# Optimization experiments

Measured on AMD Instinct MI355X. Metric: run time of the kernel, lower is better.

## Reference

```python
import jax, jax.numpy as jnp
import numpy as np

H, W = 30, 30
D = 256
MAX_OBJECTS = 16
SENT = H * W  # sentinel label for background / invalid slots


def label_components(grid):
    """4-connected same-color connected-component labeling.
    grid: [B,H,W] int32. Returns labels [B,H,W] where each foreground cell
    carries the minimum linear index of its component (== raster-scan BFS
    discovery order of the torch code), SENT for background."""
    B = grid.shape[0]
    lin = jnp.arange(H * W, dtype=jnp.int32).reshape(1, H, W)
    fg = grid > 0
    init = jnp.where(fg, lin, SENT).astype(jnp.int32)
    big = jnp.int32(SENT)

    def nbr_min(lab):
        lp = jnp.pad(lab, ((0, 0), (1, 1), (1, 1)), constant_values=SENT)
        gp = jnp.pad(grid, ((0, 0), (1, 1), (1, 1)), constant_values=-1)
        m = lab
        for di, dj in ((-1, 0), (1, 0), (0, -1), (0, 1)):
            ls = lp[:, 1 + di:1 + di + H, 1 + dj:1 + dj + W]
            gs = gp[:, 1 + di:1 + di + H, 1 + dj:1 + dj + W]
            m = jnp.minimum(m, jnp.where(gs == grid, ls, big))
        return jnp.where(fg, m, big)

    def cond(s):
        return s[1]

    def body(s):
        lab, _ = s
        new = nbr_min(lab)
        # pointer jumping: label <- min(label, label[label]) accelerates convergence
        flat = new.reshape(B, H * W)
        jumped = jnp.take_along_axis(flat, jnp.clip(flat, 0, H * W - 1), axis=1)
        flat = jnp.where(flat < SENT, jnp.minimum(flat, jumped), SENT)
        new = flat.reshape(B, H, W)
        return new, jnp.any(new != lab)

    labels, _ = jax.lax.while_loop(cond, body, (init, jnp.array(True)))
    return labels


def extract_objects(grid, labels):
    """Per-slot (color, y, x, h, w, valid), each [B, MAX_OBJECTS]."""
    B = grid.shape[0]
    HW = H * W
    lin = jnp.arange(HW, dtype=jnp.int32)
    rows, cols = lin // W, lin % W
    lab = labels.reshape(B, HW)
    ns = HW + 1  # extra segment collects background
    seg = jnp.where(lab < SENT, lab, SENT)
    rmin = jax.vmap(lambda s: jax.ops.segment_min(rows, s, num_segments=ns))(seg)
    rmax = jax.vmap(lambda s: jax.ops.segment_max(rows, s, num_segments=ns))(seg)
    cmin = jax.vmap(lambda s: jax.ops.segment_min(cols, s, num_segments=ns))(seg)
    cmax = jax.vmap(lambda s: jax.ops.segment_max(cols, s, num_segments=ns))(seg)
    # component roots, in raster order == BFS discovery order; keep first K
    root = jnp.where((lab == lin[None, :]) & (lab < SENT), lin[None, :], SENT)
    order = jnp.sort(root, axis=1)[:, :MAX_OBJECTS]
    valid = order < SENT
    idx = jnp.clip(order, 0, HW - 1)
    bi = jnp.arange(B)[:, None]
    y = jnp.clip(rmin[bi, idx], 0, H - 1)
    x = jnp.clip(cmin[bi, idx], 0, W - 1)
    y2 = jnp.clip(rmax[bi, idx] + 1, y + 1, H)
    x2 = jnp.clip(cmax[bi, idx] + 1, x + 1, W)
    color = grid.reshape(B, HW)[bi, idx]
    return color, y, x, y2 - y, x2 - x, valid


def forward(grid_emb, structure_rep, W1, b1, W2, b2, Wp, bp, gamma, beta, ortho_scale, objs):
    color, y, x, h, w, valid = objs
    B = grid_emb.shape[0]
    bi = jnp.arange(B)[:, None]
    # summed-area table -> bbox mean-pool of grid_emb in O(1) per object
    S = jnp.pad(jnp.cumsum(jnp.cumsum(grid_emb, axis=1), axis=2),
                ((0, 0), (1, 0), (1, 0), (0, 0)))
    y2, x2 = y + h, x + w
    pool = S[bi, y2, x2] - S[bi, y, x2] - S[bi, y2, x] + S[bi, y, x]
    pool = pool / (h * w).astype(grid_emb.dtype)[..., None]       # [B,K,D]
    bbox = jnp.stack([color / 9.0, x / W, y / H, w / W, h / H], axis=-1).astype(grid_emb.dtype)
    combined = jnp.concatenate([pool, bbox], axis=-1)              # [B,K,D+5]
    hdn = jax.nn.gelu(jnp.einsum('bkf,fd->bkd', combined, W1) + b1, approximate=False)
    obj = jnp.einsum('bkd,de->bke', hdn, W2) + b2
    obj = jnp.where(valid[..., None], obj, 0.0)  # pad slots are zero embeddings
    # OrthogonalProjector with structure broadcast = mean over structure slots
    s = structure_rep.mean(axis=1, keepdims=True)                  # [B,1,D]
    sn = s / jnp.maximum(jnp.linalg.norm(s, axis=-1, keepdims=True), 1e-8)
    dot = (obj * sn).sum(axis=-1, keepdims=True)
    co = (obj - dot * sn) * ortho_scale
    co = jnp.einsum('bkd,de->bke', co, Wp) + bp
    mu = co.mean(axis=-1, keepdims=True)
    var = ((co - mu) ** 2).mean(axis=-1, keepdims=True)
    return (co - mu) / jnp.sqrt(var + 1e-5) * gamma + beta


def setup_inputs() -> dict:
    key = jax.random.key(0)
    ks = jax.random.split(key, 6)
    B, K_STRUCT = 128, 8
    grid_emb = jax.random.normal(ks[0], (B, H, W, D), dtype=jnp.float32)
    grid = jax.random.randint(ks[1], (B, H, W), 0, 10, dtype=jnp.int32)
    structure_rep = jax.random.normal(ks[2], (B, K_STRUCT, D), dtype=jnp.float32)
    sc = 0.02
    W1 = jax.random.normal(ks[3], (D + 5, D), dtype=jnp.float32) * sc
    b1 = jnp.zeros((D,), jnp.float32)
    W2 = jax.random.normal(ks[4], (D, D), dtype=jnp.float32) * sc
    b2 = jnp.zeros((D,), jnp.float32)
    Wp = jax.random.normal(ks[5], (D, D), dtype=jnp.float32) * sc
    bp = jnp.zeros((D,), jnp.float32)
    gamma = jnp.ones((D,), jnp.float32)
    beta = jnp.zeros((D,), jnp.float32)
    ortho_scale = jnp.ones((1,), jnp.float32)
    return dict(grid_emb=grid_emb, grid=grid, structure_rep=structure_rep,
                W1=W1, b1=b1, W2=W2, b2=b2, Wp=Wp, bp=bp,
                gamma=gamma, beta=beta, ortho_scale=ortho_scale)


def reference(grid_emb, grid, structure_rep, W1, b1, W2, b2, Wp, bp, gamma, beta, ortho_scale):
    labels = label_components(grid)
    objs = extract_objects(grid, labels)
    return forward(grid_emb, structure_rep, W1, b1, W2, b2, Wp, bp, gamma, beta, ortho_scale, objs)
```

## Files before the change

kernel.cpp:

```cpp
#include <hip/hip_runtime.h>
#include <math.h>

#define HH 30
#define WWID 30
#define HW 900
#define SENTV 900
#define DD 256
#define MAXK 16
#define AK 264

typedef __attribute__((ext_vector_type(8))) short short8b;
typedef __attribute__((ext_vector_type(4))) float f32x4;

__device__ __forceinline__ float gelu_exact(float x) {
    return 0.5f * x * (1.0f + erff(x * 0.70710678118654752440f));
}

__device__ __forceinline__ unsigned short f2bf(float x) {
    unsigned int u = __float_as_uint(x);
    u += 0x7FFFu + ((u >> 16) & 1u);
    return (unsigned short)(u >> 16);
}

__global__ __launch_bounds__(256) void conv_w(
    const float* __restrict__ W1, const float* __restrict__ W2,
    const float* __restrict__ Wp, unsigned short* __restrict__ ws)
{
    int f = blockIdx.x * 256 + threadIdx.x;
    int m = f >> 13;
    int rem = f & 8191;
    int ntile = rem >> 9;
    int kl = rem & 511;
    int ktile = kl >> 6;
    int lane = kl & 63;
    const float* W = (m == 0) ? W1 : (m == 1) ? W2 : Wp;
    int k0 = ktile * 32 + (lane >> 4) * 8;
    int n  = ntile * 16 + (lane & 15);
    unsigned short* dst = ws + (size_t)m * 65536 +
                          ((size_t)(ntile * 8 + ktile) * 64 + lane) * 8;
    #pragma unroll
    for (int i = 0; i < 8; ++i) dst[i] = f2bf(W[(size_t)(k0 + i) * DD + n]);
}

__device__ __forceinline__ void mfma_pass16(
    const unsigned short (* __restrict__ ab)[AK],
    const unsigned short* __restrict__ wm,
    f32x4* acc, int cl, int tx, int wv)
{
    short8b afr[8];
    #pragma unroll
    for (int kt = 0; kt < 8; ++kt)
        afr[kt] = *(const short8b*)&ab[cl][kt * 32 + (tx >> 4) * 8];
    const short8b* base = (const short8b*)wm;
    short8b bfr[8];
    #pragma unroll
    for (int kt = 0; kt < 8; ++kt)
        bfr[kt] = base[(wv * 8 + kt) * 64 + tx];
    #pragma unroll
    for (int kt = 0; kt < 8; ++kt)
        *acc = __builtin_amdgcn_mfma_f32_16x16x32_bf16(afr[kt], bfr[kt], *acc, 0, 0, 0);
}

__global__ __launch_bounds__(1024, 4) void ccce_main(
    const float* __restrict__ grid_emb,
    const int* __restrict__ grid,
    const float* __restrict__ structure_rep,
    const unsigned short* __restrict__ wsw,
    const float* __restrict__ W1, const float* __restrict__ b1,
    const float* __restrict__ b2, const float* __restrict__ bp,
    const float* __restrict__ gvec, const float* __restrict__ bvec,
    const float* __restrict__ ortho_scale,
    float* __restrict__ out, int KS)
{
    const int b   = blockIdx.x;
    const int tid = threadIdx.x;
    const int tx  = tid & 63;
    const int wv  = tid >> 6;
    const int cl  = tx & 15;
    const int g   = tx >> 4;

    __shared__ int color_s[HW];
    __shared__ int lab_s[HW];
    __shared__ int slot_of[HW];
    __shared__ int root_s[MAXK];
    __shared__ int nroot_s;
    __shared__ int by0[MAXK], by1[MAXK], bx0[MAXK], bx1[MAXK];
    __shared__ __align__(16) unsigned short a0[16][AK];
    __shared__ __align__(16) unsigned short a1[16][AK];
    __shared__ __align__(16) float sn_s[DD];
    __shared__ float red_s[4];
    __shared__ float feats_s[16][5];
    __shared__ float dred[16][16];
    __shared__ float lred[16][16][2];

    const int4* gp = (const int4*)(grid + (size_t)b * HW);
    int4 gld;
    if (tid < 225) gld = gp[tid];

    const bool do_s = (tid < DD);
    float sl0=0.f,sl1=0.f,sl2=0.f,sl3=0.f,sl4=0.f,sl5=0.f,sl6=0.f,sl7=0.f,s_gen=0.f;
    {
        const float* sr = structure_rep + (size_t)b * KS * DD + tid;
        if (do_s) {
            if (KS == 8) {
                sl0 = sr[0*DD]; sl1 = sr[1*DD]; sl2 = sr[2*DD]; sl3 = sr[3*DD];
                sl4 = sr[4*DD]; sl5 = sr[5*DD]; sl6 = sr[6*DD]; sl7 = sr[7*DD];
            } else {
                for (int j = 0; j < KS; ++j) s_gen += sr[(size_t)j * DD];
            }
        }
    }

    if (tid < 225) {
        int i = tid * 4;
        color_s[i+0] = gld.x; lab_s[i+0] = (gld.x > 0) ? (i+0) : SENTV;
        color_s[i+1] = gld.y; lab_s[i+1] = (gld.y > 0) ? (i+1) : SENTV;
        color_s[i+2] = gld.z; lab_s[i+2] = (gld.z > 0) ? (i+2) : SENTV;
        color_s[i+3] = gld.w; lab_s[i+3] = (gld.w > 0) ? (i+3) : SENTV;
    }
    __syncthreads();

    const int li = tid;
    int nm = 0;
    if (li < HW) {
        int c = color_s[li];
        if (c > 0) {
            int r = li / WWID, cc = li - (li / WWID) * WWID;
            nm = 16;
            if (r > 0       && color_s[li - WWID] == c) nm |= 1;
            if (r < HH - 1  && color_s[li + WWID] == c) nm |= 2;
            if (cc > 0      && color_s[li - 1]    == c) nm |= 4;
            if (cc < WWID-1 && color_s[li + 1]    == c) nm |= 8;
        }
    }

    for (;;) {
        if (nm & 16) {
            int m = lab_s[li];
            if (nm & 1) m = min(m, lab_s[li - WWID]);
            if (nm & 2) m = min(m, lab_s[li + WWID]);
            if (nm & 4) m = min(m, lab_s[li - 1]);
            if (nm & 8) m = min(m, lab_s[li + 1]);
            m = min(m, lab_s[m]);
            m = min(m, lab_s[m]);
            if (m < lab_s[li]) lab_s[li] = m;
        }
        __syncthreads();
        int ch = 0;
        if (nm & 16) {
            int m = lab_s[li];
            if (nm & 1) m = min(m, lab_s[li - WWID]);
            if (nm & 2) m = min(m, lab_s[li + WWID]);
            if (nm & 4) m = min(m, lab_s[li - 1]);
            if (nm & 8) m = min(m, lab_s[li + 1]);
            m = min(m, lab_s[m]);
            m = min(m, lab_s[m]);
            if (m < lab_s[li]) { lab_s[li] = m; ch = 1; }
        }
        if (__syncthreads_count(ch) == 0) break;
    }

    if (tid < 64) {
        int base = 0;
        for (int chk = 0; chk < 15; ++chk) {
            int cell = chk * 64 + tid;
            bool isr = (cell < HW) && (color_s[cell] > 0) && (lab_s[cell] == cell);
            unsigned long long mask = __ballot(isr);
            int rank = base + __popcll(mask & ((1ull << tid) - 1ull));
            if (isr && rank < MAXK) root_s[rank] = cell;
            base += __popcll(mask);
        }
        if (tid == 0) nroot_s = base;
    } else {
        for (int i = tid - 64; i < HW; i += 960) slot_of[i] = -1;
        if (tid >= 960 && tid < 960 + MAXK) {
            int k = tid - 960;
            by0[k] = HH; by1[k] = -1; bx0[k] = WWID; bx1[k] = -1;
        }
    }
    __syncthreads();

    const int nval = min(nroot_s, MAXK);
    if (tid < nval) slot_of[root_s[tid]] = tid;
    __syncthreads();

    if (nm & 16) {
        int s = slot_of[lab_s[li]];
        if (s >= 0) {
            int r = li / WWID, cc = li - (li / WWID) * WWID;
            atomicMin(&by0[s], r); atomicMax(&by1[s], r);
            atomicMin(&bx0[s], cc); atomicMax(&bx1[s], cc);
        }
    }

    float s_mean = (KS == 8)
        ? (sl0 + sl1 + sl2 + sl3 + sl4 + sl5 + sl6 + sl7) * 0.125f
        : s_gen * (1.0f / (float)KS);
    {
        float ss = s_mean * s_mean;
        #pragma unroll
        for (int off = 32; off > 0; off >>= 1) ss += __shfl_xor(ss, off);
        if (tx == 0 && wv < 4) red_s[wv] = ss;
    }
    __syncthreads();

    if (do_s) {
        float nrm = sqrtf(red_s[0] + red_s[1] + red_s[2] + red_s[3]);
        sn_s[tid] = s_mean / fmaxf(nrm, 1e-8f);
    }

    {
        const int slot = wv;
        const int v_ok = (slot < nval) ? 1 : 0;
        const int c0 = tx * 4;
        float4 pv = make_float4(0.f, 0.f, 0.f, 0.f);
        int y = 0, x = 0, h = 1, w = 1, col = 0;
        if (v_ok) {
            y = by0[slot]; x = bx0[slot];
            h = by1[slot] + 1 - y; w = bx1[slot] + 1 - x;
            col = color_s[root_s[slot]];
            const int n = h * w;
            const float* bp_ = grid_emb + ((size_t)(b * HH + y) * WWID + x) * DD + c0;
            float4 sum = make_float4(0.f, 0.f, 0.f, 0.f);
            for (int base2 = 0; base2 < n; base2 += 8) {
                float4 v[8];
                #pragma unroll
                for (int t = 0; t < 8; ++t) {
                    int ii = base2 + t;
                    if (ii < n) {
                        int yy = ii / w, xx = ii - yy * w;
                        v[t] = *(const float4*)(bp_ + ((size_t)yy * WWID + xx) * DD);
                    }
                }
                #pragma unroll
                for (int t = 0; t < 8; ++t) {
                    int ii = base2 + t;
                    if (ii < n) { sum.x += v[t].x; sum.y += v[t].y; sum.z += v[t].z; sum.w += v[t].w; }
                }
            }
            float inv = 1.0f / (float)n;
            pv.x = sum.x * inv; pv.y = sum.y * inv; pv.z = sum.z * inv; pv.w = sum.w * inv;
        }
        unsigned int p0 = (unsigned int)f2bf(pv.x) | ((unsigned int)f2bf(pv.y) << 16);
        unsigned int p1 = (unsigned int)f2bf(pv.z) | ((unsigned int)f2bf(pv.w) << 16);
        *(unsigned int*)&a0[wv][c0]     = p0;
        *(unsigned int*)&a0[wv][c0 + 2] = p1;
        if (tx < 5) {
            float f = 0.f;
            if (v_ok) {
                switch (tx) {
                    case 0: f = (float)col / 9.0f; break;
                    case 1: f = (float)x  / 30.0f; break;
                    case 2: f = (float)y  / 30.0f; break;
                    case 3: f = (float)w  / 30.0f; break;
                    case 4: f = (float)h  / 30.0f; break;
                }
            }
            feats_s[wv][tx] = f;
        }
    }
    __syncthreads();

    {
        f32x4 acc = {0, 0, 0, 0};
        mfma_pass16(a0, wsw, &acc, cl, tx, wv);
        const int col = wv * 16 + cl;
        float b1v = b1[col];
        float tw[5];
        #pragma unroll
        for (int jj = 0; jj < 5; ++jj) tw[jj] = W1[(size_t)(256 + jj) * DD + col];
        #pragma unroll
        for (int j = 0; j < 4; ++j) {
            int row = g * 4 + j;
            float s = acc[j] + b1v;
            #pragma unroll
            for (int jj = 0; jj < 5; ++jj) s += feats_s[row][jj] * tw[jj];
            a1[row][col] = f2bf(gelu_exact(s));
        }
        __syncthreads();
    }

    {
        f32x4 acc = {0, 0, 0, 0};
        mfma_pass16(a1, wsw + 65536, &acc, cl, tx, wv);
        const int col = wv * 16 + cl;
        float b2v = b2[col];
        float snc = sn_s[col];
        float obj[4];
        float pd[4];
        #pragma unroll
        for (int j = 0; j < 4; ++j) {
            int row = g * 4 + j;
            float vm = (row < nval) ? 1.f : 0.f;
            obj[j] = (acc[j] + b2v) * vm;
            pd[j] = obj[j] * snc;
        }
        #pragma unroll
        for (int off = 1; off < 16; off <<= 1) {
            #pragma unroll
            for (int j = 0; j < 4; ++j) pd[j] += __shfl_xor(pd[j], off);
        }
        if (cl == 0) {
            #pragma unroll
            for (int j = 0; j < 4; ++j) dred[wv][g * 4 + j] = pd[j];
        }
        __syncthreads();
        float osc = ortho_scale[0];
        #pragma unroll
        for (int j = 0; j < 4; ++j) {
            int row = g * 4 + j;
            float p = 0.f;
            #pragma unroll
            for (int w = 0; w < 16; ++w) p += dred[w][row];
            a0[row][col] = f2bf((obj[j] - p * snc) * osc);
        }
        __syncthreads();
    }

    {
        f32x4 acc = {0, 0, 0, 0};
        mfma_pass16(a0, wsw + 2 * 65536, &acc, cl, tx, wv);
        const int col = wv * 16 + cl;
        float bpv = bp[col];
        float v[4], S[4], Q[4];
        #pragma unroll
        for (int j = 0; j < 4; ++j) {
            v[j] = acc[j] + bpv;
            S[j] = v[j];
            Q[j] = v[j] * v[j];
        }
        #pragma unroll
        for (int off = 1; off < 16; off <<= 1) {
            #pragma unroll
            for (int j = 0; j < 4; ++j) {
                S[j] += __shfl_xor(S[j], off);
                Q[j] += __shfl_xor(Q[j], off);
            }
        }
        if (cl == 0) {
            #pragma unroll
            for (int j = 0; j < 4; ++j) {
                lred[wv][g * 4 + j][0] = S[j];
                lred[wv][g * 4 + j][1] = Q[j];
            }
        }
        __syncthreads();
        float gvc = gvec[col], bvc = bvec[col];
        #pragma unroll
        for (int j = 0; j < 4; ++j) {
            int row = g * 4 + j;
            float Ss = 0.f, Qq = 0.f;
            #pragma unroll
            for (int w = 0; w < 16; ++w) { Ss += lred[w][row][0]; Qq += lred[w][row][1]; }
            float mu   = Ss * (1.0f / 256.0f);
            float var  = fmaxf(Qq * (1.0f / 256.0f) - mu * mu, 0.0f);
            float rstd = 1.0f / sqrtf(var + 1e-5f);
            out[((size_t)(b * MAXK + row)) * DD + col] = (v[j] - mu) * rstd * gvc + bvc;
        }
    }
}

extern "C" void kernel_launch(void* const* d_in, const int* in_sizes, int n_in,
                              void* d_out, int out_size, void* d_ws, size_t ws_size,
                              hipStream_t stream) {
    const float* grid_emb = (const float*)d_in[0];
    const int*   grid     = (const int*)d_in[1];
    const float* srep     = (const float*)d_in[2];
    const float* W1v = (const float*)d_in[3];
    const float* b1v = (const float*)d_in[4];
    const float* W2v = (const float*)d_in[5];
    const float* b2v = (const float*)d_in[6];
    const float* Wpv = (const float*)d_in[7];
    const float* bpv = (const float*)d_in[8];
    const float* gv  = (const float*)d_in[9];
    const float* bv  = (const float*)d_in[10];
    const float* osv = (const float*)d_in[11];
    float* out = (float*)d_out;

    const int B  = in_sizes[1] / HW;
    const int KS = in_sizes[2] / (B * DD);

    unsigned short* wsw = (unsigned short*)d_ws;
    hipLaunchKernelGGL(conv_w, dim3(96), dim3(256), 0, stream,
                       W1v, W2v, Wpv, wsw);
    hipLaunchKernelGGL(ccce_main, dim3(B), dim3(1024), 0, stream,
                       grid_emb, grid, srep, wsw, W1v, b1v, b2v, bpv,
                       gv, bv, osv, out, KS);
}
```

Before: 27.81 us.

## Fuse weight conversion into main kernel via cooperative launch and grid sync

```diff
diff --git a/kernel.cpp b/kernel.cpp
--- a/kernel.cpp
+++ b/kernel.cpp
@@ -1,5 +1,8 @@
 #include <hip/hip_runtime.h>
+#include <hip/hip_cooperative_groups.h>
 #include <math.h>
+
+namespace cg = cooperative_groups;
 
 #define HH 30
 #define WWID 30
@@ -8,6 +11,7 @@
 #define DD 256
 #define MAXK 16
 #define AK 264
+#define NFRAG 24576
 
 typedef __attribute__((ext_vector_type(8))) short short8b;
 typedef __attribute__((ext_vector_type(4))) float f32x4;
@@ -20,26 +24,6 @@
     unsigned int u = __float_as_uint(x);
     u += 0x7FFFu + ((u >> 16) & 1u);
     return (unsigned short)(u >> 16);
-}
-
-__global__ __launch_bounds__(256) void conv_w(
-    const float* __restrict__ W1, const float* __restrict__ W2,
-    const float* __restrict__ Wp, unsigned short* __restrict__ ws)
-{
-    int f = blockIdx.x * 256 + threadIdx.x;
-    int m = f >> 13;
-    int rem = f & 8191;
-    int ntile = rem >> 9;
-    int kl = rem & 511;
-    int ktile = kl >> 6;
-    int lane = kl & 63;
-    const float* W = (m == 0) ? W1 : (m == 1) ? W2 : Wp;
-    int k0 = ktile * 32 + (lane >> 4) * 8;
-    int n  = ntile * 16 + (lane & 15);
-    unsigned short* dst = ws + (size_t)m * 65536 +
-                          ((size_t)(ntile * 8 + ktile) * 64 + lane) * 8;
-    #pragma unroll
-    for (int i = 0; i < 8; ++i) dst[i] = f2bf(W[(size_t)(k0 + i) * DD + n]);
 }
 
 __device__ __forceinline__ void mfma_pass16(
@@ -65,9 +49,11 @@
     const float* __restrict__ grid_emb,
     const int* __restrict__ grid,
     const float* __restrict__ structure_rep,
-    const unsigned short* __restrict__ wsw,
-    const float* __restrict__ W1, const float* __restrict__ b1,
-    const float* __restrict__ b2, const float* __restrict__ bp,
+    unsigned short* __restrict__ wsw,
+    const float* __restrict__ W1, const float* __restrict__ W2,
+    const float* __restrict__ Wp,
+    const float* __restrict__ b1, const float* __restrict__ b2,
+    const float* __restrict__ bp,
     const float* __restrict__ gvec, const float* __restrict__ bvec,
     const float* __restrict__ ortho_scale,
     float* __restrict__ out, int KS)
@@ -111,12 +97,45 @@
         }
     }
 
+    {
+        const int fpb = (NFRAG + gridDim.x - 1) / gridDim.x;
+        for (int t = tid; t < fpb; t += 1024) {
+            int f = b * fpb + t;
+            if (f < NFRAG) {
+                int m = f >> 13;
+                int rem = f & 8191;
+                int ntile = rem >> 9;
+                int kl = rem & 511;
+                int ktile = kl >> 6;
+                int lane = kl & 63;
+                const float* W = (m == 0) ? W1 : (m == 1) ? W2 : Wp;
+                int k0 = ktile * 32 + (lane >> 4) * 8;
+                int n  = ntile * 16 + (lane & 15);
+                const float* src = W + (size_t)k0 * DD + n;
+                float v0 = src[0*DD], v1 = src[1*DD], v2 = src[2*DD], v3 = src[3*DD];
+                float v4 = src[4*DD], v5 = src[5*DD], v6 = src[6*DD], v7 = src[7*DD];
+                short8b frag;
+                frag[0] = (short)f2bf(v0); frag[1] = (short)f2bf(v1);
+                frag[2] = (short)f2bf(v2); frag[3] = (short)f2bf(v3);
+                frag[4] = (short)f2bf(v4); frag[5] = (short)f2bf(v5);
+                frag[6] = (short)f2bf(v6); frag[7] = (short)f2bf(v7);
+                *(short8b*)(wsw + (size_t)m * 65536 +
+                            ((size_t)(ntile * 8 + ktile) * 64 + lane) * 8) = frag;
+            }
+        }
+    }
+
     if (tid < 225) {
         int i = tid * 4;
         color_s[i+0] = gld.x; lab_s[i+0] = (gld.x > 0) ? (i+0) : SENTV;
         color_s[i+1] = gld.y; lab_s[i+1] = (gld.y > 0) ? (i+1) : SENTV;
         color_s[i+2] = gld.z; lab_s[i+2] = (gld.z > 0) ? (i+2) : SENTV;
         color_s[i+3] = gld.w; lab_s[i+3] = (gld.w > 0) ? (i+3) : SENTV;
+    }
+    if (tid < HW) slot_of[tid] = -1;
+    if (tid >= 1000 && tid < 1000 + MAXK) {
+        int k = tid - 1000;
+        by0[k] = HH; by1[k] = -1; bx0[k] = WWID; bx1[k] = -1;
     }
     __syncthreads();
 
@@ -167,22 +186,14 @@
             bool isr = (cell < HW) && (color_s[cell] > 0) && (lab_s[cell] == cell);
             unsigned long long mask = __ballot(isr);
             int rank = base + __popcll(mask & ((1ull << tid) - 1ull));
-            if (isr && rank < MAXK) root_s[rank] = cell;
+            if (isr && rank < MAXK) { root_s[rank] = cell; slot_of[cell] = rank; }
             base += __popcll(mask);
         }
         if (tid == 0) nroot_s = base;
-    } else {
-        for (int i = tid - 64; i < HW; i += 960) slot_of[i] = -1;
-        if (tid >= 960 && tid < 960 + MAXK) {
-            int k = tid - 960;
-            by0[k] = HH; by1[k] = -1; bx0[k] = WWID; bx1[k] = -1;
-        }
     }
     __syncthreads();
 
     const int nval = min(nroot_s, MAXK);
-    if (tid < nval) slot_of[root_s[tid]] = tid;
-    __syncthreads();
 
     if (nm & 16) {
         int s = slot_of[lab_s[li]];
@@ -261,6 +272,9 @@
     }
     __syncthreads();
 
+    __threadfence();
+    cg::this_grid().sync();
+
     {
         f32x4 acc = {0, 0, 0, 0};
         mfma_pass16(a0, wsw, &acc, cl, tx, wv);
@@ -377,13 +391,15 @@
     const float* osv = (const float*)d_in[11];
     float* out = (float*)d_out;
 
-    const int B  = in_sizes[1] / HW;
-    const int KS = in_sizes[2] / (B * DD);
-
+    int B  = in_sizes[1] / HW;
+    int KS = in_sizes[2] / (B * DD);
     unsigned short* wsw = (unsigned short*)d_ws;
-    hipLaunchKernelGGL(conv_w, dim3(96), dim3(256), 0, stream,
-                       W1v, W2v, Wpv, wsw);
-    hipLaunchKernelGGL(ccce_main, dim3(B), dim3(1024), 0, stream,
-                       grid_emb, grid, srep, wsw, W1v, b1v, b2v, bpv,
-                       gv, bv, osv, out, KS);
+
+    void* args[] = { (void*)&grid_emb, (void*)&grid, (void*)&srep, (void*)&wsw,
+                     (void*)&W1v, (void*)&W2v, (void*)&Wpv,
+                     (void*)&b1v, (void*)&b2v, (void*)&bpv,
+                     (void*)&gv, (void*)&bv, (void*)&osv,
+                     (void*)&out, (void*)&KS };
+    hipLaunchCooperativeKernel((void*)ccce_main, dim3(B), dim3(1024),
+                               args, 0, stream);
 }
```

Measured after the change: 89.64 us. +222.4%, slower.

## Fuse weight bf16 conversion into main kernel and prefetch fragments into registers

Applied to the files above, without the earlier changes.

```diff
diff --git a/kernel.cpp b/kernel.cpp
--- a/kernel.cpp
+++ b/kernel.cpp
@@ -11,6 +11,7 @@
 
 typedef __attribute__((ext_vector_type(8))) short short8b;
 typedef __attribute__((ext_vector_type(4))) float f32x4;
+typedef __attribute__((ext_vector_type(4))) unsigned int uint4v;
 
 __device__ __forceinline__ float gelu_exact(float x) {
     return 0.5f * x * (1.0f + erff(x * 0.70710678118654752440f));
@@ -22,52 +23,58 @@
     return (unsigned short)(u >> 16);
 }
 
-__global__ __launch_bounds__(256) void conv_w(
-    const float* __restrict__ W1, const float* __restrict__ W2,
-    const float* __restrict__ Wp, unsigned short* __restrict__ ws)
+__device__ __forceinline__ unsigned int cvt_pk_bf16(float a, float b) {
+    unsigned int d;
+    asm("v_cvt_pk_bf16_f32 %0, %1, %2" : "=v"(d) : "v"(a), "v"(b));
+    return d;
+}
+
+__device__ __forceinline__ void load_wfrags(
+    const float* __restrict__ W, int wv, int cl, int g, short8b wf[8])
 {
-    int f = blockIdx.x * 256 + threadIdx.x;
-    int m = f >> 13;
-    int rem = f & 8191;
-    int ntile = rem >> 9;
-    int kl = rem & 511;
-    int ktile = kl >> 6;
-    int lane = kl & 63;
-    const float* W = (m == 0) ? W1 : (m == 1) ? W2 : Wp;
-    int k0 = ktile * 32 + (lane >> 4) * 8;
-    int n  = ntile * 16 + (lane & 15);
-    unsigned short* dst = ws + (size_t)m * 65536 +
-                          ((size_t)(ntile * 8 + ktile) * 64 + lane) * 8;
+    const float* src = W + (size_t)(g * 8) * DD + (wv * 16 + cl);
     #pragma unroll
-    for (int i = 0; i < 8; ++i) dst[i] = f2bf(W[(size_t)(k0 + i) * DD + n]);
-}
-
-__device__ __forceinline__ void mfma_pass16(
+    for (int half = 0; half < 2; ++half) {
+        float v[4][8];
+        #pragma unroll
+        for (int kt = 0; kt < 4; ++kt) {
+            #pragma unroll
+            for (int i = 0; i < 8; ++i)
+                v[kt][i] = src[(size_t)((half * 4 + kt) * 32 + i) * DD];
+        }
+        #pragma unroll
+        for (int kt = 0; kt < 4; ++kt) {
+            union { uint4v u; short8b s; } cv;
+            cv.u[0] = cvt_pk_bf16(v[kt][0], v[kt][1]);
+            cv.u[1] = cvt_pk_bf16(v[kt][2], v[kt][3]);
+            cv.u[2] = cvt_pk_bf16(v[kt][4], v[kt][5]);
+            cv.u[3] = cvt_pk_bf16(v[kt][6], v[kt][7]);
+            wf[half * 4 + kt] = cv.s;
+        }
+    }
+}
+
+__device__ __forceinline__ void mfma_pass_reg(
     const unsigned short (* __restrict__ ab)[AK],
-    const unsigned short* __restrict__ wm,
-    f32x4* acc, int cl, int tx, int wv)
+    const short8b wf[8], f32x4* acc, int cl, int g)
 {
     short8b afr[8];
     #pragma unroll
     for (int kt = 0; kt < 8; ++kt)
-        afr[kt] = *(const short8b*)&ab[cl][kt * 32 + (tx >> 4) * 8];
-    const short8b* base = (const short8b*)wm;
-    short8b bfr[8];
+        afr[kt] = *(const short8b*)&ab[cl][kt * 32 + g * 8];
     #pragma unroll
     for (int kt = 0; kt < 8; ++kt)
-        bfr[kt] = base[(wv * 8 + kt) * 64 + tx];
-    #pragma unroll
-    for (int kt = 0; kt < 8; ++kt)
-        *acc = __builtin_amdgcn_mfma_f32_16x16x32_bf16(afr[kt], bfr[kt], *acc, 0, 0, 0);
+        *acc = __builtin_amdgcn_mfma_f32_16x16x32_bf16(afr[kt], wf[kt], *acc, 0, 0, 0);
 }
 
 __global__ __launch_bounds__(1024, 4) void ccce_main(
     const float* __restrict__ grid_emb,
     const int* __restrict__ grid,
     const float* __restrict__ structure_rep,
-    const unsigned short* __restrict__ wsw,
-    const float* __restrict__ W1, const float* __restrict__ b1,
-    const float* __restrict__ b2, const float* __restrict__ bp,
+    const float* __restrict__ W1, const float* __restrict__ W2,
+    const float* __restrict__ Wp,
+    const float* __restrict__ b1, const float* __restrict__ b2,
+    const float* __restrict__ bp,
     const float* __restrict__ gvec, const float* __restrict__ bvec,
     const float* __restrict__ ortho_scale,
     float* __restrict__ out, int KS)
@@ -118,6 +125,11 @@
         color_s[i+2] = gld.z; lab_s[i+2] = (gld.z > 0) ? (i+2) : SENTV;
         color_s[i+3] = gld.w; lab_s[i+3] = (gld.w > 0) ? (i+3) : SENTV;
     }
+    if (tid < HW) slot_of[tid] = -1;
+    if (tid >= 1000 && tid < 1000 + MAXK) {
+        int k = tid - 1000;
+        by0[k] = HH; by1[k] = -1; bx0[k] = WWID; bx1[k] = -1;
+    }
     __syncthreads();
 
     const int li = tid;
@@ -134,6 +146,9 @@
         }
     }
 
+    short8b wfA[8];
+    load_wfrags(W1, wv, cl, g, wfA);
+
     for (;;) {
         if (nm & 16) {
             int m = lab_s[li];
@@ -167,22 +182,14 @@
             bool isr = (cell < HW) && (color_s[cell] > 0) && (lab_s[cell] == cell);
             unsigned long long mask = __ballot(isr);
             int rank = base + __popcll(mask & ((1ull << tid) - 1ull));
-            if (isr && rank < MAXK) root_s[rank] = cell;
+            if (isr && rank < MAXK) { root_s[rank] = cell; slot_of[cell] = rank; }
             base += __popcll(mask);
         }
         if (tid == 0) nroot_s = base;
-    } else {
-        for (int i = tid - 64; i < HW; i += 960) slot_of[i] = -1;
-        if (tid >= 960 && tid < 960 + MAXK) {
-            int k = tid - 960;
-            by0[k] = HH; by1[k] = -1; bx0[k] = WWID; bx1[k] = -1;
-        }
     }
     __syncthreads();
 
     const int nval = min(nroot_s, MAXK);
-    if (tid < nval) slot_of[root_s[tid]] = tid;
-    __syncthreads();
 
     if (nm & 16) {
         int s = slot_of[lab_s[li]];
@@ -259,11 +266,14 @@
             feats_s[wv][tx] = f;
         }
     }
+
+    short8b wfB[8];
+    load_wfrags(W2, wv, cl, g, wfB);
     __syncthreads();
 
     {
         f32x4 acc = {0, 0, 0, 0};
-        mfma_pass16(a0, wsw, &acc, cl, tx, wv);
+        mfma_pass_reg(a0, wfA, &acc, cl, g);
         const int col = wv * 16 + cl;
         float b1v = b1[col];
         float tw[5];
@@ -280,9 +290,11 @@
         __syncthreads();
     }
 
+    short8b wfC[8];
     {
         f32x4 acc = {0, 0, 0, 0};
-        mfma_pass16(a1, wsw + 65536, &acc, cl, tx, wv);
+        mfma_pass_reg(a1, wfB, &acc, cl, g);
+        load_wfrags(Wp, wv, cl, g, wfC);
         const int col = wv * 16 + cl;
         float b2v = b2[col];
         float snc = sn_s[col];
@@ -319,7 +331,7 @@
 
     {
         f32x4 acc = {0, 0, 0, 0};
-        mfma_pass16(a0, wsw + 2 * 65536, &acc, cl, tx, wv);
+        mfma_pass_reg(a0, wfC, &acc, cl, g);
         const int col = wv * 16 + cl;
         float bpv = bp[col];
         float v[4], S[4], Q[4];
@@ -380,10 +392,7 @@
     const int B  = in_sizes[1] / HW;
     const int KS = in_sizes[2] / (B * DD);
 
-    unsigned short* wsw = (unsigned short*)d_ws;
-    hipLaunchKernelGGL(conv_w, dim3(96), dim3(256), 0, stream,
-                       W1v, W2v, Wpv, wsw);
     hipLaunchKernelGGL(ccce_main, dim3(B), dim3(1024), 0, stream,
-                       grid_emb, grid, srep, wsw, W1v, b1v, b2v, bpv,
-                       gv, bv, osv, out, KS);
-}
+                       grid_emb, grid, srep, W1v, W2v, Wpv,
+                       b1v, b2v, bpv, gv, bv, osv, out, KS);
+}
```

Result: faster. 26.92 us (-3.2%).
